# Performance work log

Measured on AMD Instinct MI355X. Metric: run time of the kernel, lower is better.

The kernel has to match this reference:

```python
import jax, jax.numpy as jnp
import numpy as np

B, U, V = 4, 64, 256
IN_DIM, STATE_DIM, CODE_DIM = 768, 768, 384
NUM_HEADS, HEAD_DIM = 8, 64
INNER = NUM_HEADS * HEAD_DIM  # 512
SCALE = HEAD_DIM ** 0.5


def _ln(x, g, b, eps=1e-5):
    mu = jnp.mean(x, axis=-1, keepdims=True)
    var = jnp.var(x, axis=-1, keepdims=True)
    return (x - mu) * jax.lax.rsqrt(var + eps) * g + b


def setup_inputs() -> dict:
    key = jax.random.key(0)
    ks = jax.random.split(key, 12)
    def w(k, shape, s=0.02):
        return jax.random.normal(k, shape, jnp.float32) * s
    return {
        "receiver_states": jax.random.normal(ks[0], (B, U, STATE_DIM), jnp.float32),
        "receiver_codes": jax.random.normal(ks[1], (B, U, CODE_DIM), jnp.float32),
        "sender_states": jax.random.normal(ks[2], (B, V, IN_DIM), jnp.float32),
        "ln_r_g": jnp.ones((STATE_DIM,), jnp.float32),
        "ln_r_b": jnp.zeros((STATE_DIM,), jnp.float32),
        "ln_s_g": jnp.ones((IN_DIM,), jnp.float32),
        "ln_s_b": jnp.zeros((IN_DIM,), jnp.float32),
        "Wq": w(ks[3], (STATE_DIM, INNER)), "bq": jnp.zeros((INNER,), jnp.float32), "Wmq": w(ks[4], (CODE_DIM, STATE_DIM)),
        "Wk": w(ks[5], (IN_DIM, INNER)),   "bk": jnp.zeros((INNER,), jnp.float32), "Wmk": w(ks[6], (CODE_DIM, IN_DIM)),
        "Wv": w(ks[7], (IN_DIM, INNER)),   "bv": jnp.zeros((INNER,), jnp.float32), "Wmv": w(ks[8], (CODE_DIM, IN_DIM)),
        "We": w(ks[9], (INNER, STATE_DIM)), "be": jnp.zeros((STATE_DIM,), jnp.float32), "Wme": w(ks[10], (CODE_DIM, INNER)),
        "gamma": jnp.ones((STATE_DIM,), jnp.float32),  # LayerScale, init 1.0
    }


def reference(receiver_states, receiver_codes, sender_states,
              ln_r_g, ln_r_b, ln_s_g, ln_s_b,
              Wq, bq, Wmq, Wk, bk, Wmk, Wv, bv, Wmv, We, be, Wme, gamma):
    r = _ln(receiver_states, ln_r_g, ln_r_b)   # (b,u,ds)
    s = _ln(sender_states, ln_s_g, ln_s_b)     # (b,v,di)
    # ModFC: y = (x * (1 + ctx @ Wm)) @ W + b  (code-conditioned input modulation)
    q = (r * (1.0 + receiver_codes @ Wmq)) @ Wq + bq          # (b,u,inner)
    mk = 1.0 + receiver_codes @ Wmk                           # (b,u,di)
    mv = 1.0 + receiver_codes @ Wmv                           # (b,u,di)
    xs = s[:, :, None, :]                                     # (b,v,1,di)
    k = (xs * mk[:, None, :, :]) @ Wk + bk                    # (b,v,u,inner)
    v = (xs * mv[:, None, :, :]) @ Wv + bv                    # (b,v,u,inner)
    qh = q.reshape(B, U, NUM_HEADS, HEAD_DIM)
    kh = k.reshape(B, V, U, NUM_HEADS, HEAD_DIM)
    vh = v.reshape(B, V, U, NUM_HEADS, HEAD_DIM)
    scores = jnp.einsum('buhc,bvuhc->bhuv', qh, kh) / SCALE   # (b,h,u,v)
    weights = jax.nn.softmax(scores, axis=-1)
    msg = jnp.einsum('bhuv,bvuhc->buhc', weights, vh).reshape(B, U, INNER)
    out = (msg * (1.0 + receiver_codes @ Wme)) @ We + be      # exit ModFC -> (b,u,ds)
    out = out * gamma                                         # LayerScale
    return receiver_states + out                              # residual
```

## Files before the change

### kernel.cpp

```cpp
#include <hip/hip_runtime.h>


#define DD 768
#define CDIM 384
#define NH 8
#define HD 64
#define INNER 512
#define VV 256

__device__ __forceinline__ float4 ldf4(const float* p) {
  return *(const float4*)(p);
}

__device__ __forceinline__ void fma4(float4& a, float s, const float4& b) {
  a.x += s * b.x; a.y += s * b.y; a.z += s * b.z; a.w += s * b.w;
}

__device__ __forceinline__ void fma_chunk8(const float* __restrict__ Aw,
                                           int lda, int kk, const float4* b,
                                           float4* acc) {
#pragma unroll
  for (int rg = 0; rg < 4; rg++) {
    const float* ap = Aw + (rg * 2) * lda + kk;
    float4 a0l = ldf4(ap);
    float4 a0h = ldf4(ap + 4);
    float4 a1l = ldf4(ap + lda);
    float4 a1h = ldf4(ap + lda + 4);
    float4* ac = acc + rg * 2;
    fma4(ac[0], a0l.x, b[0]); fma4(ac[1], a1l.x, b[0]);
    fma4(ac[0], a0l.y, b[1]); fma4(ac[1], a1l.y, b[1]);
    fma4(ac[0], a0l.z, b[2]); fma4(ac[1], a1l.z, b[2]);
    fma4(ac[0], a0l.w, b[3]); fma4(ac[1], a1l.w, b[3]);
    fma4(ac[0], a0h.x, b[4]); fma4(ac[1], a1h.x, b[4]);
    fma4(ac[0], a0h.y, b[5]); fma4(ac[1], a1h.y, b[5]);
    fma4(ac[0], a0h.z, b[6]); fma4(ac[1], a1h.z, b[6]);
    fma4(ac[0], a0h.w, b[7]); fma4(ac[1], a1h.w, b[7]);
  }
}

template <int KQ, int NS>
__device__ __forceinline__ void gcore8(const float* __restrict__ Aw, int lda,
                                       const float* __restrict__ Bp,
                                       float4* acc) {
  float4 b0[8], b1[8];
  const float* Bq = Bp;
#pragma unroll
  for (int i = 0; i < 8; i++) b0[i] = ldf4(Bq + (size_t)i * NS);
  Bq += (size_t)8 * NS;
#pragma unroll 1
  for (int kk = 0; kk + 16 <= KQ; kk += 16) {
#pragma unroll
    for (int i = 0; i < 8; i++) b1[i] = ldf4(Bq + (size_t)i * NS);
    Bq += (size_t)8 * NS;
    fma_chunk8(Aw, lda, kk, b0, acc);
    if (kk + 16 < KQ) {
#pragma unroll
      for (int i = 0; i < 8; i++) b0[i] = ldf4(Bq + (size_t)i * NS);
      Bq += (size_t)8 * NS;
    }
    fma_chunk8(Aw, lda, kk + 8, b1, acc);
  }
}

__device__ __forceinline__ void kred(float4* acc, float* RED, int wid,
                                     int kl) {
  __syncthreads();
  float4* R4 = (float4*)RED;
  int rg = wid & 1, kh = wid >> 1;
  if (kh) {
#pragma unroll
    for (int r = 0; r < 8; r++) R4[(rg * 8 + r) * 64 + kl] = acc[r];
  }
  __syncthreads();
  if (!kh) {
#pragma unroll
    for (int r = 0; r < 8; r++) {
      float4 v = R4[(rg * 8 + r) * 64 + kl];
      acc[r].x += v.x; acc[r].y += v.y; acc[r].z += v.z; acc[r].w += v.w;
    }
  }
}

__global__ __launch_bounds__(256, 2) void k_s1(
    const float* __restrict__ ss, const float* __restrict__ rs,
    const float* __restrict__ g_s, const float* __restrict__ b_s,
    const float* __restrict__ g_r, const float* __restrict__ b_r,
    const float* __restrict__ codes, const float* __restrict__ Wmq,
    const float* __restrict__ Wmk, const float* __restrict__ Wmv,
    const float* __restrict__ Wme, const float* __restrict__ Wk,
    float* __restrict__ s_ln, float* __restrict__ r_ln,
    float* __restrict__ cp, float* __restrict__ WkT) {
  __shared__ __align__(16) float SB[6144];
  int bid = blockIdx.x, t = threadIdx.x;
  if (bid < 176) {
    int nc = bid % 11, mb = bid / 11;
    int base = nc * 256;
    const float* W; int N, colW;
    if (base < 768)       { W = Wmq; N = DD;    colW = base; }
    else if (base < 1536) { W = Wmk; N = DD;    colW = base - 768; }
    else if (base < 2304) { W = Wmv; N = DD;    colW = base - 1536; }
    else                  { W = Wme; N = INNER; colW = base - 2304; }
    int m0 = mb * 16;
#pragma unroll
    for (int p = 0; p < 24; p++) {
      int idx = p * 256 + t, r = idx / 384, k = idx % 384;
      SB[idx] = codes[(size_t)(m0 + r) * CDIM + k];
    }
    __syncthreads();
    int kl = t & 63, wid = t >> 6, rg = wid & 1, kh = wid >> 1;
    float4 acc[8] = {};
    const float* Aw = SB + (rg * 8) * 384 + kh * 192;
    if (N == DD)
      gcore8<192, DD>(Aw, 384, W + (size_t)(kh * 192) * DD + colW + 4 * kl, acc);
    else
      gcore8<192, INNER>(Aw, 384, W + (size_t)(kh * 192) * INNER + colW + 4 * kl, acc);
    kred(acc, SB, wid, kl);
    if (!kh) {
      int gcol = base + 4 * kl;
#pragma unroll
      for (int j = 0; j < 8; j++)
        *(float4*)(cp + (size_t)(m0 + rg * 8 + j) * 2816 + gcol) = acc[j];
    }
  } else if (bid < 272) {
    int tid = bid - 176;
    int d0 = (tid >> 3) * 64, c0 = (tid & 7) * 64;
    int j = t & 63, i0 = t >> 6;
#pragma unroll
    for (int p = 0; p < 16; p++) {
      int i = p * 4 + i0;
      SB[i * 65 + j] = Wk[(size_t)(d0 + i) * INNER + c0 + j];
    }
    __syncthreads();
#pragma unroll
    for (int p = 0; p < 16; p++) {
      int i = p * 4 + i0;
      WkT[(size_t)(c0 + i) * DD + d0 + j] = SB[j * 65 + i];
    }
  } else {
    int rr = (bid - 272) * 4 + (t >> 6);
    const float *x, *g, *bb; float* y; int r;
    if (rr < 1024) { x = ss; g = g_s; bb = b_s; y = s_ln; r = rr; }
    else           { x = rs; g = g_r; bb = b_r; y = r_ln; r = rr - 1024; }
    const float* xr = x + (size_t)r * DD;
    int lane = t & 63;
    float v[12];
    float s = 0.f, sq = 0.f;
#pragma unroll
    for (int j = 0; j < 12; j++) {
      v[j] = xr[lane + 64 * j];
      s += v[j]; sq += v[j] * v[j];
    }
    for (int o = 32; o > 0; o >>= 1) {
      s += __shfl_down(s, o, 64); sq += __shfl_down(sq, o, 64);
    }
    s = __shfl(s, 0, 64); sq = __shfl(sq, 0, 64);
    float mu = s * (1.0f / 768.0f);
    float var = sq * (1.0f / 768.0f) - mu * mu;
    float rstd = rsqrtf(var + 1e-5f);
    float* yr = y + (size_t)r * DD;
#pragma unroll
    for (int j = 0; j < 12; j++) {
      int d = lane + 64 * j;
      yr[d] = (v[j] - mu) * rstd * g[d] + bb[d];
    }
  }
}

__global__ __launch_bounds__(256, 2) void k_s2(
    const float* __restrict__ s_ln, const float* __restrict__ r_ln,
    const float* __restrict__ cp, const float* __restrict__ Wq,
    float* __restrict__ sT, float* __restrict__ qp) {
  __shared__ __align__(16) float SB[4160];
  int bid = blockIdx.x, t = threadIdx.x;
  if (bid < 128) {
    int ks = bid & 3, tile = bid >> 2, nc = tile & 1, mb = tile >> 1;
    int m0 = mb * 16, col0 = nc * 256, k0 = ks * 192;
#pragma unroll
    for (int p = 0; p < 12; p++) {
      int idx = p * 256 + t, r = idx / 192, k = idx % 192;
      int d = k0 + k;
      float mqv = cp[(size_t)(m0 + r) * 2816 + d] + 1.0f;
      SB[idx] = r_ln[(size_t)(m0 + r) * DD + d] * mqv;
    }
    __syncthreads();
    int kl = t & 63, wid = t >> 6, rg = wid & 1, kh = wid >> 1;
    int col = col0 + 4 * kl;
    float4 acc[8] = {};
    gcore8<96, INNER>(SB + (rg * 8) * 192 + kh * 96, 192,
                      Wq + (size_t)(k0 + kh * 96) * INNER + col, acc);
    kred(acc, SB, wid, kl);
    if (!kh) {
      float* dst = qp + (size_t)ks * (256 * INNER);
#pragma unroll
      for (int j = 0; j < 8; j++)
        *(float4*)(dst + (size_t)(m0 + rg * 8 + j) * INNER + col) = acc[j];
    }
  } else {
    int tid = bid - 128;
    int vt = tid & 3, dt = (tid >> 2) % 12, b = tid / 48;
    int v0 = vt * 64, d0 = dt * 64;
    int j = t & 63, i0 = t >> 6;
#pragma unroll
    for (int p = 0; p < 16; p++) {
      int i = p * 4 + i0;
      SB[i * 65 + j] = s_ln[(size_t)(b * VV + v0 + i) * DD + d0 + j];
    }
    __syncthreads();
#pragma unroll
    for (int p = 0; p < 16; p++) {
      int i = p * 4 + i0;
      sT[((size_t)b * DD + d0 + i) * VV + v0 + j] = SB[j * 65 + i];
    }
  }
}

__global__ __launch_bounds__(256, 2) void k_s34(
    const float* __restrict__ qp, const float* __restrict__ bq,
    const float* __restrict__ WkT, const float* __restrict__ cp,
    const float* __restrict__ bk, const float* __restrict__ sT,
    float* __restrict__ scp, float* __restrict__ qbk) {
  __shared__ __align__(16) float SB[4096];
  int bid = blockIdx.x, t = threadIdx.x;
  int mb = bid & 15, h = (bid >> 4) & 7, ks = bid >> 7;
  int m0 = mb * 16, b = mb >> 2, k0 = ks * 256;
  {
    int r = t >> 4, c4 = (t & 15) * 4;
    int i = h * HD + c4;
    size_t off = (size_t)(m0 + r) * INNER + i;
    float4 q0 = ldf4(qp + off), q1 = ldf4(qp + 131072 + off);
    float4 q2 = ldf4(qp + 262144 + off), q3 = ldf4(qp + 393216 + off);
    float4 bq4 = ldf4(bq + i);
    float4 s;
    s.x = q0.x + q1.x + q2.x + q3.x + bq4.x;
    s.y = q0.y + q1.y + q2.y + q3.y + bq4.y;
    s.z = q0.z + q1.z + q2.z + q3.z + bq4.z;
    s.w = q0.w + q1.w + q2.w + q3.w + bq4.w;
    ((float4*)SB)[t] = s;
  }
  __syncthreads();
  if (ks == 0) {
    int m = t >> 4, cg = t & 15;
    const float* bkh = bk + h * HD;
    float p = 0.f;
#pragma unroll
    for (int c = 4 * cg; c < 4 * cg + 4; c++) p += SB[m * HD + c] * bkh[c];
    SB[1024 + t] = p;
  }
  __syncthreads();
  if (ks == 0 && t < 16) {
    float a = 0.f;
#pragma unroll
    for (int i = 0; i < 16; i++) a += SB[1024 + t * 16 + i];
    qbk[(m0 + t) * NH + h] = a;
  }
  int kl = t & 63, wid = t >> 6, rg = wid & 1, kh = wid >> 1;
  float4 acc[8] = {};
  gcore8<32, DD>(SB + (rg * 8) * HD + kh * 32, HD,
                 WkT + (size_t)(h * HD + kh * 32) * DD + k0 + 4 * kl, acc);
  kred(acc, SB, wid, kl);
  __syncthreads();
  if (!kh) {
#pragma unroll
    for (int j = 0; j < 8; j++) {
      int m = m0 + rg * 8 + j;
      const float* mkp = cp + (size_t)m * 2816 + 768 + k0 + 4 * kl;
      float4 o = {acc[j].x * (mkp[0] + 1.0f), acc[j].y * (mkp[1] + 1.0f),
                  acc[j].z * (mkp[2] + 1.0f), acc[j].w * (mkp[3] + 1.0f)};
      *(float4*)(SB + (rg * 8 + j) * 256 + 4 * kl) = o;
    }
  }
  __syncthreads();
  float4 acc2[8] = {};
  gcore8<128, VV>(SB + (rg * 8) * 256 + kh * 128, 256,
                  sT + ((size_t)b * DD + k0 + kh * 128) * VV + 4 * kl, acc2);
  kred(acc2, SB, wid, kl);
  if (!kh) {
    float* dst = scp + (size_t)ks * (2048 * VV);
#pragma unroll
    for (int j = 0; j < 8; j++) {
      int gi = (m0 + rg * 8 + j) * NH + h;
      *(float4*)(dst + (size_t)gi * VV + 4 * kl) = acc2[j];
    }
  }
}

__global__ __launch_bounds__(256, 2) void k_s5(
    const float* __restrict__ scp, const float* __restrict__ qbk,
    const float* __restrict__ s_ln, const float* __restrict__ cp,
    float* __restrict__ wsm) {
  __shared__ __align__(16) float SC[4096];
  int bid = blockIdx.x, t = threadIdx.x;
  int dc = bid % 3, up = (bid / 3) % 32, b = bid / 96;
  int gi0 = b * 512 + up * 16;
  float4* SC4 = (float4*)SC;
#pragma unroll
  for (int p = 0; p < 4; p++) {
    int idx4 = p * 256 + t;
    int r = idx4 >> 6, c4 = (idx4 & 63) * 4;
    size_t o = (size_t)(gi0 + r) * VV + c4;
    float4 v0 = ldf4(scp + o), v1 = ldf4(scp + 524288 + o);
    float4 v2 = ldf4(scp + 1048576 + o);
    int m = b * 64 + up * 2 + (r >> 3), h = r & 7;
    float qb = qbk[m * NH + h];
    float4 s;
    s.x = (v0.x + v1.x + v2.x + qb) * 0.125f;
    s.y = (v0.y + v1.y + v2.y + qb) * 0.125f;
    s.z = (v0.z + v1.z + v2.z + qb) * 0.125f;
    s.w = (v0.w + v1.w + v2.w + qb) * 0.125f;
    SC4[idx4] = s;
  }
  __syncthreads();
  int wid = t >> 6, lane = t & 63;
#pragma unroll
  for (int j = 0; j < 4; j++) {
    int r = wid * 4 + j;
    float x0 = SC[r * 256 + lane],       x1 = SC[r * 256 + lane + 64];
    float x2 = SC[r * 256 + lane + 128], x3 = SC[r * 256 + lane + 192];
    float mx = fmaxf(fmaxf(x0, x1), fmaxf(x2, x3));
    for (int o = 1; o < 64; o <<= 1) mx = fmaxf(mx, __shfl_xor(mx, o, 64));
    float e0 = __expf(x0 - mx), e1 = __expf(x1 - mx);
    float e2 = __expf(x2 - mx), e3 = __expf(x3 - mx);
    float sm = e0 + e1 + e2 + e3;
    for (int o = 1; o < 64; o <<= 1) sm += __shfl_xor(sm, o, 64);
    float rinv = 1.0f / sm;
    SC[r * 256 + lane] = e0 * rinv;       SC[r * 256 + lane + 64] = e1 * rinv;
    SC[r * 256 + lane + 128] = e2 * rinv; SC[r * 256 + lane + 192] = e3 * rinv;
  }
  __syncthreads();
  int kl = t & 63, rg = wid & 1, kh = wid >> 1;
  int col = dc * 256 + 4 * kl;
  float4 acc[8] = {};
  gcore8<128, DD>(SC + (rg * 8) * 256 + kh * 128, 256,
                  s_ln + (size_t)(b * VV + kh * 128) * DD + col, acc);
  kred(acc, SC, wid, kl);
  if (!kh) {
#pragma unroll
    for (int j = 0; j < 8; j++) {
      int m = b * 64 + up * 2 + rg;
      const float* mvp = cp + (size_t)m * 2816 + 1536 + col;
      float4 o = {acc[j].x * (mvp[0] + 1.0f), acc[j].y * (mvp[1] + 1.0f),
                  acc[j].z * (mvp[2] + 1.0f), acc[j].w * (mvp[3] + 1.0f)};
      *(float4*)(wsm + ((size_t)j * 256 + m) * DD + col) = o;
    }
  }
}

__global__ __launch_bounds__(256, 2) void k_s6(
    const float* __restrict__ wsm, const float* __restrict__ Wv,
    float* __restrict__ mmp) {
  __shared__ __align__(16) float AL[6144];
  int bid = blockIdx.x, t = threadIdx.x;
  int hp = bid & 1, ks = (bid >> 1) & 7, mb = bid >> 4;
  int h0 = hp * 4, m0 = mb * 16, k0 = ks * 96;
#pragma unroll
  for (int p = 0; p < 24; p++) {
    int idx = p * 256 + t;
    int e = idx / 1536, rem = idx % 1536, r = rem / 96, k = rem % 96;
    AL[idx] = wsm[((size_t)(h0 + e) * 256 + m0 + r) * DD + k0 + k];
  }
  __syncthreads();
  int kl = t & 63, wid = t >> 6, rg = wid & 1, kh = wid >> 1;
  int hs = kl >> 4, c4 = 4 * (kl & 15);
  int colg = h0 * HD + hs * HD + c4;
  const float* Aw = AL + hs * 1536 + (rg * 8) * 96 + kh * 48;
  float4 acc[8] = {};
  gcore8<48, INNER>(Aw, 96, Wv + (size_t)(k0 + kh * 48) * INNER + colg, acc);
  kred(acc, AL, wid, kl);
  if (!kh) {
    float* dst = mmp + (size_t)ks * (256 * INNER);
#pragma unroll
    for (int j = 0; j < 8; j++)
      *(float4*)(dst + (size_t)(m0 + rg * 8 + j) * INNER + colg) = acc[j];
  }
}

__global__ __launch_bounds__(256, 2) void k_s7(
    const float* __restrict__ mmp, const float* __restrict__ bvv,
    const float* __restrict__ cp, const float* __restrict__ We,
    float* __restrict__ op) {
  __shared__ __align__(16) float AL[4096];
  int bid = blockIdx.x, t = threadIdx.x;
  int ks = bid & 7, dc = (bid >> 3) % 3, mb = bid / 24;
  int m0 = mb * 16, k0 = ks * 64;
  {
    int r = t >> 4, k4 = (t & 15) * 4;
    int i = k0 + k4;
    size_t off = (size_t)(m0 + r) * INNER + i;
    float4 v = ldf4(mmp + off);
    float4 m1 = ldf4(mmp + 131072 + off), m2 = ldf4(mmp + 262144 + off);
    float4 m3 = ldf4(mmp + 393216 + off), m4 = ldf4(mmp + 524288 + off);
    float4 m5 = ldf4(mmp + 655360 + off), m6 = ldf4(mmp + 786432 + off);
    float4 m7 = ldf4(mmp + 917504 + off);
    v.x = v.x + m1.x + m2.x + m3.x + m4.x + m5.x + m6.x + m7.x;
    v.y = v.y + m1.y + m2.y + m3.y + m4.y + m5.y + m6.y + m7.y;
    v.z = v.z + m1.z + m2.z + m3.z + m4.z + m5.z + m6.z + m7.z;
    v.w = v.w + m1.w + m2.w + m3.w + m4.w + m5.w + m6.w + m7.w;
    float4 me = ldf4(cp + (size_t)(m0 + r) * 2816 + 2304 + i);
    float4 bv4 = ldf4(bvv + i);
    float4 res = {(v.x + bv4.x) * (me.x + 1.0f), (v.y + bv4.y) * (me.y + 1.0f),
                  (v.z + bv4.z) * (me.z + 1.0f), (v.w + bv4.w) * (me.w + 1.0f)};
    ((float4*)AL)[t] = res;
  }
  __syncthreads();
  int kl = t & 63, wid = t >> 6, rg = wid & 1, kh = wid >> 1;
  int col = dc * 256 + 4 * kl;
  float4 acc[8] = {};
  gcore8<32, DD>(AL + (rg * 8) * 64 + kh * 32, 64,
                 We + (size_t)(k0 + kh * 32) * DD + col, acc);
  kred(acc, AL, wid, kl);
  if (!kh) {
    float* dst = op + (size_t)ks * (256 * DD);
#pragma unroll
    for (int j = 0; j < 8; j++)
      *(float4*)(dst + (size_t)(m0 + rg * 8 + j) * DD + col) = acc[j];
  }
}

__global__ __launch_bounds__(256, 2) void k_s8(
    const float* __restrict__ op, const float* __restrict__ be,
    const float* __restrict__ gamma, const float* __restrict__ rs,
    float* __restrict__ outp) {
  int m = blockIdx.x, t = threadIdx.x;
  if (t < 192) {
    int d = 4 * t;
    size_t off = (size_t)m * DD + d;
    float4 v = ldf4(op + off);
    float4 o1 = ldf4(op + 196608 + off), o2 = ldf4(op + 393216 + off);
    float4 o3 = ldf4(op + 589824 + off), o4 = ldf4(op + 786432 + off);
    float4 o5 = ldf4(op + 983040 + off), o6 = ldf4(op + 1179648 + off);
    float4 o7 = ldf4(op + 1376256 + off);
    v.x = v.x + o1.x + o2.x + o3.x + o4.x + o5.x + o6.x + o7.x;
    v.y = v.y + o1.y + o2.y + o3.y + o4.y + o5.y + o6.y + o7.y;
    v.z = v.z + o1.z + o2.z + o3.z + o4.z + o5.z + o6.z + o7.z;
    v.w = v.w + o1.w + o2.w + o3.w + o4.w + o5.w + o6.w + o7.w;
    float4 bev = ldf4(be + d), gv = ldf4(gamma + d);
    float4 rv = ldf4(rs + off);
    float4 out = {rv.x + (v.x + bev.x) * gv.x, rv.y + (v.y + bev.y) * gv.y,
                  rv.z + (v.z + bev.z) * gv.z, rv.w + (v.w + bev.w) * gv.w};
    *(float4*)(outp + off) = out;
  }
}

extern "C" void kernel_launch(void* const* d_in, const int* in_sizes, int n_in,
                              void* d_out, int out_size, void* d_ws, size_t ws_size,
                              hipStream_t stream) {
  const float* rs     = (const float*)d_in[0];
  const float* codes  = (const float*)d_in[1];
  const float* ss     = (const float*)d_in[2];
  const float* ln_r_g = (const float*)d_in[3];
  const float* ln_r_b = (const float*)d_in[4];
  const float* ln_s_g = (const float*)d_in[5];
  const float* ln_s_b = (const float*)d_in[6];
  const float* Wq  = (const float*)d_in[7];
  const float* bq  = (const float*)d_in[8];
  const float* Wk  = (const float*)d_in[10];
  const float* bk  = (const float*)d_in[11];
  const float* Wmq = (const float*)d_in[9];
  const float* Wmk = (const float*)d_in[12];
  const float* Wv  = (const float*)d_in[13];
  const float* bv  = (const float*)d_in[14];
  const float* Wmv = (const float*)d_in[15];
  const float* We  = (const float*)d_in[16];
  const float* be  = (const float*)d_in[17];
  const float* Wme = (const float*)d_in[18];
  const float* gamma = (const float*)d_in[19];

  float* w = (float*)d_ws;
  float* s_ln = w;
  float* r_ln = w + 786432;
  float* WkT  = w + 983040;
  float* qp   = w + 1376256;
  float* sT   = w + 1900544;
  float* cp   = w + 2686976;
  float* qbk  = w + 3407872;
  float* qm   = w + 3409920;
  float* scp  = w + 4982784;
  float* wsm  = qm;
  float* mmp  = r_ln;
  float* op   = scp;

  k_s1<<<dim3(592), 256, 0, stream>>>(ss, rs, ln_s_g, ln_s_b, ln_r_g, ln_r_b,
                                      codes, Wmq, Wmk, Wmv, Wme, Wk,
                                      s_ln, r_ln, cp, WkT);
  k_s2<<<dim3(320), 256, 0, stream>>>(s_ln, r_ln, cp, Wq, sT, qp);
  k_s34<<<dim3(384), 256, 0, stream>>>(qp, bq, WkT, cp, bk, sT, scp, qbk);
  k_s5<<<dim3(384), 256, 0, stream>>>(scp, qbk, s_ln, cp, wsm);
  k_s6<<<dim3(256), 256, 0, stream>>>(wsm, Wv, mmp);
  k_s7<<<dim3(384), 256, 0, stream>>>(mmp, bv, cp, We, op);
  k_s8<<<dim3(256), 256, 0, stream>>>(op, be, gamma, rs, (float*)d_out);
}
```

Before: 179.9 us.

## Fuse exit projection and residual epilogue, drop split-K partials

Merges the exit ModFC GEMM and the final bias/LayerScale/residual kernel into a single kernel. Each block now covers the full K=512 reduction for a 16-row by 256-column tile, so the 8-way split-K partial buffer and the reduction pass over it are gone. This saves a kernel launch and the round trip of the partial outputs through global memory. In exchange the grid shrinks from 384 blocks to 48, each doing a long serial K loop, which can leave most of the GPU's compute units idle.

```diff
diff --git a/kernel.cpp b/kernel.cpp
--- a/kernel.cpp
+++ b/kernel.cpp
@@ -374,17 +374,19 @@
   }
 }
 
-__global__ __launch_bounds__(256, 2) void k_s7(
+__global__ __launch_bounds__(256, 2) void k_s78(
     const float* __restrict__ mmp, const float* __restrict__ bvv,
     const float* __restrict__ cp, const float* __restrict__ We,
-    float* __restrict__ op) {
-  __shared__ __align__(16) float AL[4096];
-  int bid = blockIdx.x, t = threadIdx.x;
-  int ks = bid & 7, dc = (bid >> 3) % 3, mb = bid / 24;
-  int m0 = mb * 16, k0 = ks * 64;
-  {
-    int r = t >> 4, k4 = (t & 15) * 4;
-    int i = k0 + k4;
+    const float* __restrict__ be, const float* __restrict__ gamma,
+    const float* __restrict__ rs, float* __restrict__ outp) {
+  __shared__ __align__(16) float AL[8192];
+  int bid = blockIdx.x, t = threadIdx.x;
+  int mb = bid & 15, dc = bid >> 4;
+  int m0 = mb * 16, col0 = dc * 256;
+#pragma unroll
+  for (int p = 0; p < 8; p++) {
+    int idx4 = p * 256 + t;
+    int r = idx4 >> 7, i = (idx4 & 127) * 4;
     size_t off = (size_t)(m0 + r) * INNER + i;
     float4 v = ldf4(mmp + off);
     float4 m1 = ldf4(mmp + 131072 + off), m2 = ldf4(mmp + 262144 + off);
@@ -399,45 +401,28 @@
     float4 bv4 = ldf4(bvv + i);
     float4 res = {(v.x + bv4.x) * (me.x + 1.0f), (v.y + bv4.y) * (me.y + 1.0f),
                   (v.z + bv4.z) * (me.z + 1.0f), (v.w + bv4.w) * (me.w + 1.0f)};
-    ((float4*)AL)[t] = res;
+    ((float4*)AL)[idx4] = res;
   }
   __syncthreads();
   int kl = t & 63, wid = t >> 6, rg = wid & 1, kh = wid >> 1;
-  int col = dc * 256 + 4 * kl;
+  int col = col0 + 4 * kl;
   float4 acc[8] = {};
-  gcore8<32, DD>(AL + (rg * 8) * 64 + kh * 32, 64,
-                 We + (size_t)(k0 + kh * 32) * DD + col, acc);
+  gcore8<256, DD>(AL + (rg * 8) * INNER + kh * 256, INNER,
+                  We + (size_t)(kh * 256) * DD + col, acc);
   kred(acc, AL, wid, kl);
   if (!kh) {
-    float* dst = op + (size_t)ks * (256 * DD);
-#pragma unroll
-    for (int j = 0; j < 8; j++)
-      *(float4*)(dst + (size_t)(m0 + rg * 8 + j) * DD + col) = acc[j];
-  }
-}
-
-__global__ __launch_bounds__(256, 2) void k_s8(
-    const float* __restrict__ op, const float* __restrict__ be,
-    const float* __restrict__ gamma, const float* __restrict__ rs,
-    float* __restrict__ outp) {
-  int m = blockIdx.x, t = threadIdx.x;
-  if (t < 192) {
-    int d = 4 * t;
-    size_t off = (size_t)m * DD + d;
-    float4 v = ldf4(op + off);
-    float4 o1 = ldf4(op + 196608 + off), o2 = ldf4(op + 393216 + off);
-    float4 o3 = ldf4(op + 589824 + off), o4 = ldf4(op + 786432 + off);
-    float4 o5 = ldf4(op + 983040 + off), o6 = ldf4(op + 1179648 + off);
-    float4 o7 = ldf4(op + 1376256 + off);
-    v.x = v.x + o1.x + o2.x + o3.x + o4.x + o5.x + o6.x + o7.x;
-    v.y = v.y + o1.y + o2.y + o3.y + o4.y + o5.y + o6.y + o7.y;
-    v.z = v.z + o1.z + o2.z + o3.z + o4.z + o5.z + o6.z + o7.z;
-    v.w = v.w + o1.w + o2.w + o3.w + o4.w + o5.w + o6.w + o7.w;
-    float4 bev = ldf4(be + d), gv = ldf4(gamma + d);
-    float4 rv = ldf4(rs + off);
-    float4 out = {rv.x + (v.x + bev.x) * gv.x, rv.y + (v.y + bev.y) * gv.y,
-                  rv.z + (v.z + bev.z) * gv.z, rv.w + (v.w + bev.w) * gv.w};
-    *(float4*)(outp + off) = out;
+    float4 bev = ldf4(be + col), gv = ldf4(gamma + col);
+#pragma unroll
+    for (int j = 0; j < 8; j++) {
+      int m = m0 + rg * 8 + j;
+      size_t off = (size_t)m * DD + col;
+      float4 rv = ldf4(rs + off);
+      float4 o = {rv.x + (acc[j].x + bev.x) * gv.x,
+                  rv.y + (acc[j].y + bev.y) * gv.y,
+                  rv.z + (acc[j].z + bev.z) * gv.z,
+                  rv.w + (acc[j].w + bev.w) * gv.w};
+      *(float4*)(outp + off) = o;
+    }
   }
 }
 
@@ -477,7 +462,6 @@
   float* scp  = w + 4982784;
   float* wsm  = qm;
   float* mmp  = r_ln;
-  float* op   = scp;
 
   k_s1<<<dim3(592), 256, 0, stream>>>(ss, rs, ln_s_g, ln_s_b, ln_r_g, ln_r_b,
                                       codes, Wmq, Wmk, Wmv, Wme, Wk,
@@ -486,6 +470,6 @@
   k_s34<<<dim3(384), 256, 0, stream>>>(qp, bq, WkT, cp, bk, sT, scp, qbk);
   k_s5<<<dim3(384), 256, 0, stream>>>(scp, qbk, s_ln, cp, wsm);
   k_s6<<<dim3(256), 256, 0, stream>>>(wsm, Wv, mmp);
-  k_s7<<<dim3(384), 256, 0, stream>>>(mmp, bv, cp, We, op);
-  k_s8<<<dim3(256), 256, 0, stream>>>(op, be, gamma, rs, (float*)d_out);
-}
+  k_s78<<<dim3(48), 256, 0, stream>>>(mmp, bv, cp, We, be, gamma, rs,
+                                      (float*)d_out);
+}
```

Measured after the change: 190.5 us. +5.9%, slower.
